# Kernel optimization log

Measured on AMD Instinct MI355X. Metric: run time of the kernel, lower is better.

## Reference

```python
import jax, jax.numpy as jnp
import numpy as np

B, T, C = 2, 2048, 2048
H, D, G = 16, 128, 4   # num_heads, head_dim, num_kv_groups
EPS = 1e-6


def setup_inputs() -> dict:
    key = jax.random.key(0)
    ks = jax.random.split(key, 6)
    x = jax.random.normal(ks[0], (B, T, C), dtype=jnp.float32)
    # causal mask: True = disallowed (strictly upper triangular)
    mask = jnp.triu(jnp.ones((T, T), dtype=bool), k=1)
    # RoPE tables, full head_dim with duplicated angle halves
    inv_freq = 1.0 / (10000.0 ** (jnp.arange(0, D, 2, dtype=jnp.float32) / D))
    angles = jnp.arange(T, dtype=jnp.float32)[:, None] * inv_freq[None, :]  # [T, D/2]
    angles = jnp.concatenate([angles, angles], axis=-1)                     # [T, D]
    cos, sin = jnp.cos(angles), jnp.sin(angles)
    std = 0.02
    W_query = jax.random.normal(ks[1], (C, H * D), dtype=jnp.float32) * std
    W_key = jax.random.normal(ks[2], (C, G * D), dtype=jnp.float32) * std
    W_value = jax.random.normal(ks[3], (C, G * D), dtype=jnp.float32) * std
    W_out = jax.random.normal(ks[4], (H * D, C), dtype=jnp.float32) * std
    q_scale = jnp.ones((D,), dtype=jnp.float32)
    k_scale = jnp.ones((D,), dtype=jnp.float32)
    return {"x": x, "mask": mask, "cos": cos, "sin": sin,
            "W_query": W_query, "W_key": W_key, "W_value": W_value,
            "W_out": W_out, "q_scale": q_scale, "k_scale": k_scale}


def _rmsnorm(x, scale):
    # qwen3-compatible: compute in fp32, rescale, cast back
    xf = x.astype(jnp.float32)
    var = jnp.mean(xf * xf, axis=-1, keepdims=True)
    return (xf * jax.lax.rsqrt(var + EPS) * scale).astype(x.dtype)


def _rope(x, cos, sin):
    d = x.shape[-1]
    x1, x2 = x[..., : d // 2], x[..., d // 2 :]
    rotated = jnp.concatenate([-x2, x1], axis=-1)
    # cos/sin: [T, D] -> broadcast over [B, H, T, D]
    return (x * cos[None, None] + rotated * sin[None, None]).astype(x.dtype)


def reference(x, mask, cos, sin, W_query, W_key, W_value, W_out, q_scale, k_scale):
    b, t, _ = x.shape
    Q = (x @ W_query).reshape(b, t, H, D).transpose(0, 2, 1, 3)  # [B,H,T,D]
    K = (x @ W_key).reshape(b, t, G, D).transpose(0, 2, 1, 3)    # [B,G,T,D]
    V = (x @ W_value).reshape(b, t, G, D).transpose(0, 2, 1, 3)
    group_size = H // G
    K = jnp.repeat(K, group_size, axis=1)  # [B,H,T,D]
    V = jnp.repeat(V, group_size, axis=1)
    Q = _rmsnorm(Q, q_scale)
    K = _rmsnorm(K, k_scale)
    Q = _rope(Q, cos, sin)
    K = _rope(K, cos, sin)
    scale = D ** (-0.5)
    attn = jnp.einsum("bhqd,bhkd->bhqk", Q, K) * scale
    attn = jnp.where(mask[None, None], -jnp.inf, attn)
    w = jax.nn.softmax(attn, axis=-1)
    out = jnp.einsum("bhqk,bhkd->bhqd", w, V)
    out = out.transpose(0, 2, 1, 3).reshape(b, t, H * D)
    return out @ W_out
```

## Files before the change

kernel.cpp:

```cpp
#include <hip/hip_runtime.h>
#include <hip/hip_bf16.h>

#define Bq 2
#define Tt 2048
#define Cc 2048
#define Hh 16
#define Dd 128
#define Gg 4

using bf16 = __hip_bfloat16;
typedef __attribute__((ext_vector_type(8))) short short8;
typedef __attribute__((ext_vector_type(4))) float f32x4;

__device__ __forceinline__ void gload_lds16(const void* g, void* l) {
    __builtin_amdgcn_global_load_lds(
        (const __attribute__((address_space(1))) unsigned int*)g,
        (__attribute__((address_space(3))) unsigned int*)l, 16, 0, 0);
}

__global__ void k_cast_bf16(const float* __restrict__ in, bf16* __restrict__ out, int n4) {
    int i = blockIdx.x * blockDim.x + threadIdx.x;
    if (i >= n4) return;
    float4 v = ((const float4*)in)[i];
    union { bf16 h[4]; uint2 u; } u;
    u.h[0] = __float2bfloat16(v.x);
    u.h[1] = __float2bfloat16(v.y);
    u.h[2] = __float2bfloat16(v.z);
    u.h[3] = __float2bfloat16(v.w);
    ((uint2*)out)[i] = u.u;
}

__global__ void k_cast_transpose(const float* __restrict__ in, bf16* __restrict__ out,
                                 int rows, int cols, int ostride) {
    __shared__ float tile[32][33];
    int c0 = blockIdx.x * 32, r0 = blockIdx.y * 32;
    int tx = threadIdx.x, ty = threadIdx.y;
    #pragma unroll
    for (int k = 0; k < 4; ++k)
        tile[ty + 8*k][tx] = in[(size_t)(r0 + ty + 8*k) * cols + c0 + tx];
    __syncthreads();
    #pragma unroll
    for (int k = 0; k < 4; ++k)
        out[(size_t)(c0 + ty + 8*k) * ostride + r0 + tx] = __float2bfloat16(tile[tx][ty + 8*k]);
}

__global__ void k_vt(const bf16* __restrict__ QKV, bf16* __restrict__ Vt) {
    __shared__ bf16 tile[64][65];
    const int d0 = blockIdx.x * 64, t0 = blockIdx.y * 64;
    const int bg = blockIdx.z;
    const int b = bg >> 2, g = bg & 3;
    const int tx = threadIdx.x, ty = threadIdx.y;
    const bf16* src = QKV + (size_t)(b * Tt) * 3072 + 2560 + g * 128;
    #pragma unroll
    for (int k = 0; k < 8; ++k)
        tile[ty + 8*k][tx] = src[(size_t)(t0 + ty + 8*k) * 3072 + d0 + tx];
    __syncthreads();
    bf16* dst = Vt + (size_t)bg * Dd * Tt;
    #pragma unroll
    for (int k = 0; k < 8; ++k)
        dst[(size_t)(d0 + ty + 8*k) * Tt + t0 + tx] = tile[tx][ty + 8*k];
}

template<int OUTF32>
__global__ __launch_bounds__(512, 2)
void k_gemm8(const bf16* __restrict__ A, const bf16* __restrict__ Bt,
             void* __restrict__ C, int M, int N, int K, int nbx) {
    __shared__ __align__(16) bf16 As[2][256 * 64];
    __shared__ __align__(16) bf16 Bs[2][256 * 64];
    const int tid = threadIdx.x;
    const int lane = tid & 63;
    const int wid = tid >> 6;
    const int wm = wid >> 2, wn = wid & 3;

    const int nb = gridDim.x;
    const int cpx = nb >> 3;
    const int id = blockIdx.x;
    const int sid = (id & 7) * cpx + (id >> 3);
    const int bx = sid % nbx, by = sid / nbx;
    const int row0 = by * 256, col0 = bx * 256;

    const int srow = tid >> 3;
    const int NT = K >> 6;

    f32x4 acc[8][4] = {};

#define STAGE_A(bufq, tt, c) {                                              \
        const int r_ = (c) * 64 + srow;                                     \
        const int ch_ = (tid & 7) ^ (r_ & 7);                               \
        gload_lds16(A + (size_t)(row0 + r_) * K + (tt) * 64 + ch_ * 8,      \
                    &As[bufq][(c) * 4096 + wid * 512]); }
#define STAGE_B(bufq, tt, c) {                                              \
        const int r_ = (c) * 64 + srow;                                     \
        const int ch_ = (tid & 7) ^ (r_ & 7);                               \
        gload_lds16(Bt + (size_t)(col0 + r_) * K + (tt) * 64 + ch_ * 8,     \
                    &Bs[bufq][(c) * 4096 + wid * 512]); }

    #pragma unroll
    for (int c = 0; c < 4; ++c) STAGE_A(0, 0, c);
    #pragma unroll
    for (int c = 0; c < 4; ++c) STAGE_B(0, 0, c);

    for (int t = 0; t < NT; ++t) {
        const int p = t & 1, q = p ^ 1;
        const bf16* a = As[p];
        const bf16* bm = Bs[p];
        const bool pf = (t + 1 < NT);

        auto rdA = [&](int i, int kk) -> short8 {
            const int ra = wm * 128 + i * 16 + (lane & 15);
            return *(const short8*)((const char*)a + ra * 128 +
                   ((kk * 64 + (lane >> 4) * 16) ^ ((ra & 7) << 4)));
        };
        auto rdB = [&](int j, int kk) -> short8 {
            const int rb = wn * 64 + j * 16 + (lane & 15);
            return *(const short8*)((const char*)bm + rb * 128 +
                   ((kk * 64 + (lane >> 4) * 16) ^ ((rb & 7) << 4)));
        };

        if (pf) { STAGE_A(q, t + 1, 0); STAGE_A(q, t + 1, 1); }
        if (pf) asm volatile("s_waitcnt vmcnt(2)" ::: "memory");
        else    asm volatile("s_waitcnt vmcnt(0)" ::: "memory");
        __builtin_amdgcn_s_barrier();
        asm volatile("" ::: "memory");

        short8 af[4][2];
        #pragma unroll
        for (int i = 0; i < 4; ++i)
            #pragma unroll
            for (int kk = 0; kk < 2; ++kk) af[i][kk] = rdA(i, kk);
        {
            short8 bf0[2][2];
            #pragma unroll
            for (int j = 0; j < 2; ++j)
                #pragma unroll
                for (int kk = 0; kk < 2; ++kk) bf0[j][kk] = rdB(j, kk);
            __builtin_amdgcn_s_setprio(1);
            #pragma unroll
            for (int i = 0; i < 4; ++i)
                #pragma unroll
                for (int j = 0; j < 2; ++j)
                    #pragma unroll
                    for (int kk = 0; kk < 2; ++kk)
                        acc[i][j] = __builtin_amdgcn_mfma_f32_16x16x32_bf16(af[i][kk], bf0[j][kk], acc[i][j], 0, 0, 0);
            __builtin_amdgcn_s_setprio(0);
        }
        asm volatile("" ::: "memory");
        __builtin_amdgcn_s_barrier();

        {
            short8 bf1[2][2];
            #pragma unroll
            for (int j = 0; j < 2; ++j)
                #pragma unroll
                for (int kk = 0; kk < 2; ++kk) bf1[j][kk] = rdB(j + 2, kk);
            if (pf) { STAGE_A(q, t + 1, 2); STAGE_A(q, t + 1, 3); }
            asm volatile("" ::: "memory");
            __builtin_amdgcn_s_barrier();
            __builtin_amdgcn_s_setprio(1);
            #pragma unroll
            for (int i = 0; i < 4; ++i)
                #pragma unroll
                for (int j = 0; j < 2; ++j)
                    #pragma unroll
                    for (int kk = 0; kk < 2; ++kk)
                        acc[i][j + 2] = __builtin_amdgcn_mfma_f32_16x16x32_bf16(af[i][kk], bf1[j][kk], acc[i][j + 2], 0, 0, 0);
            __builtin_amdgcn_s_setprio(0);
        }
        asm volatile("" ::: "memory");
        __builtin_amdgcn_s_barrier();

        short8 ag[4][2];
        #pragma unroll
        for (int i = 0; i < 4; ++i)
            #pragma unroll
            for (int kk = 0; kk < 2; ++kk) ag[i][kk] = rdA(i + 4, kk);
        {
            short8 bf0[2][2];
            #pragma unroll
            for (int j = 0; j < 2; ++j)
                #pragma unroll
                for (int kk = 0; kk < 2; ++kk) bf0[j][kk] = rdB(j, kk);
            if (pf) { STAGE_B(q, t + 1, 0); STAGE_B(q, t + 1, 1); }
            asm volatile("" ::: "memory");
            __builtin_amdgcn_s_barrier();
            __builtin_amdgcn_s_setprio(1);
            #pragma unroll
            for (int i = 0; i < 4; ++i)
                #pragma unroll
                for (int j = 0; j < 2; ++j)
                    #pragma unroll
                    for (int kk = 0; kk < 2; ++kk)
                        acc[i + 4][j] = __builtin_amdgcn_mfma_f32_16x16x32_bf16(ag[i][kk], bf0[j][kk], acc[i + 4][j], 0, 0, 0);
            __builtin_amdgcn_s_setprio(0);
        }
        asm volatile("" ::: "memory");
        __builtin_amdgcn_s_barrier();

        {
            short8 bf1[2][2];
            #pragma unroll
            for (int j = 0; j < 2; ++j)
                #pragma unroll
                for (int kk = 0; kk < 2; ++kk) bf1[j][kk] = rdB(j + 2, kk);
            if (pf) { STAGE_B(q, t + 1, 2); STAGE_B(q, t + 1, 3); }
            asm volatile("" ::: "memory");
            __builtin_amdgcn_s_barrier();
            __builtin_amdgcn_s_setprio(1);
            #pragma unroll
            for (int i = 0; i < 4; ++i)
                #pragma unroll
                for (int j = 0; j < 2; ++j)
                    #pragma unroll
                    for (int kk = 0; kk < 2; ++kk)
                        acc[i + 4][j + 2] = __builtin_amdgcn_mfma_f32_16x16x32_bf16(ag[i][kk], bf1[j][kk], acc[i + 4][j + 2], 0, 0, 0);
            __builtin_amdgcn_s_setprio(0);
        }
        asm volatile("" ::: "memory");
        __builtin_amdgcn_s_barrier();
    }
#undef STAGE_A
#undef STAGE_B

    const int crow0 = row0 + wm * 128 + (lane >> 4) * 4;
    const int ccol0 = col0 + wn * 64 + (lane & 15);
    #pragma unroll
    for (int i = 0; i < 8; ++i)
        #pragma unroll
        for (int j = 0; j < 4; ++j)
            #pragma unroll
            for (int r = 0; r < 4; ++r) {
                const size_t idx = (size_t)(crow0 + i * 16 + r) * N + ccol0 + j * 16;
                const float v = acc[i][j][r];
                if (OUTF32) ((float*)C)[idx] = v;
                else        ((bf16*)C)[idx] = __float2bfloat16(v);
            }
}

__global__ void k_qkv_post(const bf16* __restrict__ QKV,
                           const float* __restrict__ cosT, const float* __restrict__ sinT,
                           const float* __restrict__ qs, const float* __restrict__ ks,
                           bf16* __restrict__ Qr, bf16* __restrict__ Kr) {
    const int bt = blockIdx.x;
    const int b = bt >> 11;
    const int t = bt & 2047;
    const int lane = threadIdx.x & 63;
    const int wave = threadIdx.x >> 6;
    const float c1 = cosT[t * 128 + lane],      c2 = cosT[t * 128 + 64 + lane];
    const float s1 = sinT[t * 128 + lane],      s2 = sinT[t * 128 + 64 + lane];
    const float qs1 = qs[lane], qs2 = qs[lane + 64];
    const float ks1 = ks[lane], ks2 = ks[lane + 64];
    const bf16* rowb = QKV + (size_t)bt * 3072;
    for (int rr = wave; rr < 20; rr += 4) {
        const bf16* src = rowb + rr * 128;
        const float x1 = __bfloat162float(src[lane]);
        const float x2 = __bfloat162float(src[lane + 64]);
        bf16* dst;
        if (rr < 16) dst = Qr + ((size_t)(b * Hh + rr) * Tt + t) * 128;
        else         dst = Kr + ((size_t)(b * Gg + (rr - 16)) * Tt + t) * 128;
        float ssum = x1 * x1 + x2 * x2;
        #pragma unroll
        for (int o = 32; o > 0; o >>= 1) ssum += __shfl_xor(ssum, o);
        const float inv = rsqrtf(ssum * (1.0f / 128.0f) + 1e-6f);
        const float post = (rr < 16) ? 0.08838834764831845f : 1.0f;
        const float sc1 = ((rr < 16) ? qs1 : ks1) * inv;
        const float sc2 = ((rr < 16) ? qs2 : ks2) * inv;
        const float y1 = x1 * sc1;
        const float y2 = x2 * sc2;
        dst[lane]      = __float2bfloat16((y1 * c1 - y2 * s1) * post);
        dst[lane + 64] = __float2bfloat16((y2 * c2 + y1 * s2) * post);
    }
}

__global__ __launch_bounds__(256)
void k_attn(const bf16* __restrict__ Qr, const bf16* __restrict__ Kr,
            const bf16* __restrict__ Vt, bf16* __restrict__ AO) {
    __shared__ __align__(16) bf16 Ksm[2][64 * 128];
    __shared__ __align__(16) bf16 Vsm[2][128 * 64];
    __shared__ __align__(16) bf16 Psm[4][16 * 64];
    const int id = blockIdx.x;
    const int bg = id & 7;
    const int wid = id >> 3;
    const int pair = wid & 15;
    const int hg = wid >> 4;
    const int b = bg >> 2, g = bg & 3;
    const int h = g * 4 + hg;
    const int lane = threadIdx.x & 63;
    const int wave = threadIdx.x >> 6;

    const bf16* Kbase = Kr + (size_t)(b * Gg + g) * Tt * Dd;
    const bf16* Vbase = Vt + (size_t)(b * Gg + g) * Dd * Tt;

    for (int pass = 0; pass < 2; ++pass) {
        const int qt = pass ? (31 - pair) : pair;
        const bf16* Qbase = Qr + ((size_t)(b * Hh + h) * Tt + qt * 64) * Dd;

        short8 qf[4];
        #pragma unroll
        for (int kk = 0; kk < 4; ++kk)
            qf[kk] = *(const short8*)(Qbase + (size_t)(wave * 16 + (lane & 15)) * 128 + kk * 32 + (lane >> 4) * 8);

        float l_run[4] = {0.f, 0.f, 0.f, 0.f};
        f32x4 oacc[8];
        #pragma unroll
        for (int j = 0; j < 8; ++j) oacc[j] = (f32x4){0.f, 0.f, 0.f, 0.f};

        {
            #pragma unroll
            for (int j = 0; j < 4; ++j) {
                const int c = j * 4 + wave;
                const int rtk = c * 4 + (lane >> 4);
                const int chk = (lane & 15) ^ (rtk & 7);
                gload_lds16(Kbase + (size_t)rtk * 128 + chk * 8, Ksm[0] + c * 512);
                const int rtv = c * 8 + (lane >> 3);
                const int chv = (lane & 7) ^ ((lane >> 3) & 7);
                gload_lds16(Vbase + (size_t)rtv * Tt + chv * 8, Vsm[0] + c * 512);
            }
        }

        int cur = 0;
        for (int tk = 0; tk <= qt; ++tk) {
            __syncthreads();

            if (tk < qt) {
                const int k0n = (tk + 1) * 64;
                #pragma unroll
                for (int j = 0; j < 4; ++j) {
                    const int c = j * 4 + wave;
                    const int rtk = c * 4 + (lane >> 4);
                    const int chk = (lane & 15) ^ (rtk & 7);
                    gload_lds16(Kbase + (size_t)(k0n + rtk) * 128 + chk * 8, Ksm[cur ^ 1] + c * 512);
                    const int rtv = c * 8 + (lane >> 3);
                    const int chv = (lane & 7) ^ ((lane >> 3) & 7);
                    gload_lds16(Vbase + (size_t)rtv * Tt + k0n + chv * 8, Vsm[cur ^ 1] + c * 512);
                }
            }

            const bf16* Ks = Ksm[cur];
            const bf16* Vs = Vsm[cur];

            f32x4 s[4];
            #pragma unroll
            for (int nt = 0; nt < 4; ++nt) s[nt] = (f32x4){0.f, 0.f, 0.f, 0.f};
            __builtin_amdgcn_s_setprio(1);
            #pragma unroll
            for (int nt = 0; nt < 4; ++nt) {
                #pragma unroll
                for (int kk = 0; kk < 4; ++kk) {
                    const int rk = nt * 16 + (lane & 15);
                    short8 kf = *(const short8*)((const char*)Ks + rk * 256 +
                                ((kk * 64 + (lane >> 4) * 16) ^ ((rk & 7) << 4)));
                    s[nt] = __builtin_amdgcn_mfma_f32_16x16x32_bf16(qf[kk], kf, s[nt], 0, 0, 0);
                }
            }
            __builtin_amdgcn_s_setprio(0);

            if (tk == qt) {
                const int qrow = qt * 64 + wave * 16 + (lane >> 4) * 4;
                const int k0 = tk * 64;
                #pragma unroll
                for (int nt = 0; nt < 4; ++nt) {
                    const int kcol = k0 + nt * 16 + (lane & 15);
                    #pragma unroll
                    for (int r = 0; r < 4; ++r)
                        if (kcol > qrow + r) s[nt][r] = -1e30f;
                }
            }

            #pragma unroll
            for (int nt = 0; nt < 4; ++nt)
                #pragma unroll
                for (int r = 0; r < 4; ++r) {
                    const float p = __expf(s[nt][r]);
                    l_run[r] += p;
                    s[nt][r] = p;
                }

            #pragma unroll
            for (int nt = 0; nt < 4; ++nt)
                #pragma unroll
                for (int r = 0; r < 4; ++r) {
                    const int prow = (lane >> 4) * 4 + r;
                    const int pcol = nt * 16 + (lane & 15);
                    *(bf16*)((char*)Psm[wave] + ((prow * 128 + pcol * 2) ^ ((prow & 7) << 4))) =
                        __float2bfloat16(s[nt][r]);
                }
            #pragma unroll
            for (int kk = 0; kk < 2; ++kk) {
                const int pr = lane & 15;
                short8 pf = *(const short8*)((const char*)Psm[wave] + pr * 128 +
                            ((kk * 64 + (lane >> 4) * 16) ^ ((pr & 7) << 4)));
                __builtin_amdgcn_s_setprio(1);
                #pragma unroll
                for (int j = 0; j < 8; ++j) {
                    const int rb = j * 16 + (lane & 15);
                    short8 vf = *(const short8*)((const char*)Vs + rb * 128 +
                                ((kk * 64 + (lane >> 4) * 16) ^ ((rb & 7) << 4)));
                    oacc[j] = __builtin_amdgcn_mfma_f32_16x16x32_bf16(pf, vf, oacc[j], 0, 0, 0);
                }
                __builtin_amdgcn_s_setprio(0);
            }
            cur ^= 1;
        }
        __syncthreads();

        #pragma unroll
        for (int o = 1; o < 16; o <<= 1)
            #pragma unroll
            for (int r = 0; r < 4; ++r) l_run[r] += __shfl_xor(l_run[r], o);

        #pragma unroll
        for (int r = 0; r < 4; ++r) {
            const float inv = 1.0f / l_run[r];
            const int qrow = qt * 64 + wave * 16 + (lane >> 4) * 4 + r;
            bf16* dst = AO + (size_t)(b * Tt + qrow) * 2048 + h * 128 + (lane & 15);
            #pragma unroll
            for (int j = 0; j < 8; ++j)
                dst[j * 16] = __float2bfloat16(oacc[j][r] * inv);
        }
    }
}

extern "C" void kernel_launch(void* const* d_in, const int* in_sizes, int n_in,
                              void* d_out, int out_size, void* d_ws, size_t ws_size,
                              hipStream_t stream) {
    const float* x    = (const float*)d_in[0];
    const float* cosT = (const float*)d_in[2];
    const float* sinT = (const float*)d_in[3];
    const float* Wq   = (const float*)d_in[4];
    const float* Wk   = (const float*)d_in[5];
    const float* Wv   = (const float*)d_in[6];
    const float* Wo   = (const float*)d_in[7];
    const float* qs   = (const float*)d_in[8];
    const float* ks   = (const float*)d_in[9];

    char* ws = (char*)d_ws;
    bf16* xb   = (bf16*)(ws);
    bf16* Wcat = (bf16*)(ws + 16777216);
    bf16* Wot  = (bf16*)(ws + 29360128);
    bf16* QKV  = (bf16*)(ws + 37748736);
    bf16* Qr   = (bf16*)(ws + 62914560);
    bf16* Kr   = (bf16*)(ws + 79691776);
    bf16* Vtp  = (bf16*)(ws + 83886080);
    bf16* AO   = (bf16*)(ws + 88080384);

    k_cast_bf16<<<8192, 256, 0, stream>>>(x, xb, 2097152);
    dim3 tb(32, 8);
    k_cast_transpose<<<dim3(64, 64), tb, 0, stream>>>(Wq, Wcat, 2048, 2048, 2048);
    k_cast_transpose<<<dim3(16, 64), tb, 0, stream>>>(Wk, Wcat + (size_t)2048 * 2048, 2048, 512, 2048);
    k_cast_transpose<<<dim3(16, 64), tb, 0, stream>>>(Wv, Wcat + (size_t)2560 * 2048, 2048, 512, 2048);
    k_cast_transpose<<<dim3(64, 64), tb, 0, stream>>>(Wo, Wot, 2048, 2048, 2048);

    k_gemm8<0><<<192, 512, 0, stream>>>(xb, Wcat, QKV, 4096, 3072, 2048, 12);
    k_qkv_post<<<4096, 256, 0, stream>>>(QKV, cosT, sinT, qs, ks, Qr, Kr);
    k_vt<<<dim3(2, 32, 8), dim3(64, 8), 0, stream>>>(QKV, Vtp);
    k_attn<<<512, 256, 0, stream>>>(Qr, Kr, Vtp, AO);
    k_gemm8<1><<<128, 512, 0, stream>>>(AO, Wot, d_out, 4096, 2048, 2048, 8);
}
```

Before: 237.0 us.

## Narrow GEMM N-tile to raise block count and simplify the pipeline loop

The bf16 GEMM kernel is templated on the N-tile width (NJF*64 columns). The QKV projection now uses 256x192 tiles over 256 blocks instead of 256x256 over 192, and the output projection uses 256x128 over 256 blocks instead of 128. The K-loop is also restructured: the whole next tile is prefetched at the top, all B fragments are loaded once, and then four groups of A rows are processed with a barrier after each. This is meant to fill more of the CUs and cut the barrier and interleaving overhead. In exchange, each block does less MFMA work per loaded byte, and the single wait at the top of the loop overlaps global loads with compute less tightly.

```diff
diff --git a/kernel.cpp b/kernel.cpp
--- a/kernel.cpp
+++ b/kernel.cpp
@@ -61,12 +61,12 @@
         dst[(size_t)(d0 + ty + 8*k) * Tt + t0 + tx] = tile[tx][ty + 8*k];
 }
 
-template<int OUTF32>
+template<int OUTF32, int NJF>
 __global__ __launch_bounds__(512, 2)
 void k_gemm8(const bf16* __restrict__ A, const bf16* __restrict__ Bt,
              void* __restrict__ C, int M, int N, int K, int nbx) {
     __shared__ __align__(16) bf16 As[2][256 * 64];
-    __shared__ __align__(16) bf16 Bs[2][256 * 64];
+    __shared__ __align__(16) bf16 Bs[2][NJF * 64 * 64];
     const int tid = threadIdx.x;
     const int lane = tid & 63;
     const int wid = tid >> 6;
@@ -77,12 +77,12 @@
     const int id = blockIdx.x;
     const int sid = (id & 7) * cpx + (id >> 3);
     const int bx = sid % nbx, by = sid / nbx;
-    const int row0 = by * 256, col0 = bx * 256;
+    const int row0 = by * 256, col0 = bx * (NJF * 64);
 
     const int srow = tid >> 3;
     const int NT = K >> 6;
 
-    f32x4 acc[8][4] = {};
+    f32x4 acc[8][NJF] = {};
 
 #define STAGE_A(bufq, tt, c) {                                              \
         const int r_ = (c) * 64 + srow;                                     \
@@ -98,13 +98,25 @@
     #pragma unroll
     for (int c = 0; c < 4; ++c) STAGE_A(0, 0, c);
     #pragma unroll
-    for (int c = 0; c < 4; ++c) STAGE_B(0, 0, c);
+    for (int c = 0; c < NJF; ++c) STAGE_B(0, 0, c);
 
     for (int t = 0; t < NT; ++t) {
         const int p = t & 1, q = p ^ 1;
         const bf16* a = As[p];
         const bf16* bm = Bs[p];
         const bool pf = (t + 1 < NT);
+
+        if (pf) {
+            #pragma unroll
+            for (int c = 0; c < 4; ++c) STAGE_A(q, t + 1, c);
+            #pragma unroll
+            for (int c = 0; c < NJF; ++c) STAGE_B(q, t + 1, c);
+            asm volatile("s_waitcnt vmcnt(%0)" :: "i"(4 + NJF) : "memory");
+        } else {
+            asm volatile("s_waitcnt vmcnt(0)" ::: "memory");
+        }
+        __builtin_amdgcn_s_barrier();
+        asm volatile("" ::: "memory");
 
         auto rdA = [&](int i, int kk) -> short8 {
             const int ra = wm * 128 + i * 16 + (lane & 15);
@@ -112,121 +124,47 @@
                    ((kk * 64 + (lane >> 4) * 16) ^ ((ra & 7) << 4)));
         };
         auto rdB = [&](int j, int kk) -> short8 {
-            const int rb = wn * 64 + j * 16 + (lane & 15);
+            const int rb = wn * (NJF * 16) + j * 16 + (lane & 15);
             return *(const short8*)((const char*)bm + rb * 128 +
                    ((kk * 64 + (lane >> 4) * 16) ^ ((rb & 7) << 4)));
         };
 
-        if (pf) { STAGE_A(q, t + 1, 0); STAGE_A(q, t + 1, 1); }
-        if (pf) asm volatile("s_waitcnt vmcnt(2)" ::: "memory");
-        else    asm volatile("s_waitcnt vmcnt(0)" ::: "memory");
-        __builtin_amdgcn_s_barrier();
-        asm volatile("" ::: "memory");
-
-        short8 af[4][2];
-        #pragma unroll
-        for (int i = 0; i < 4; ++i)
-            #pragma unroll
-            for (int kk = 0; kk < 2; ++kk) af[i][kk] = rdA(i, kk);
-        {
-            short8 bf0[2][2];
-            #pragma unroll
-            for (int j = 0; j < 2; ++j)
-                #pragma unroll
-                for (int kk = 0; kk < 2; ++kk) bf0[j][kk] = rdB(j, kk);
+        short8 bfr[NJF][2];
+        #pragma unroll
+        for (int j = 0; j < NJF; ++j)
+            #pragma unroll
+            for (int kk = 0; kk < 2; ++kk) bfr[j][kk] = rdB(j, kk);
+
+        #pragma unroll
+        for (int g = 0; g < 4; ++g) {
+            short8 af[2][2];
+            #pragma unroll
+            for (int ii = 0; ii < 2; ++ii)
+                #pragma unroll
+                for (int kk = 0; kk < 2; ++kk) af[ii][kk] = rdA(g * 2 + ii, kk);
             __builtin_amdgcn_s_setprio(1);
             #pragma unroll
-            for (int i = 0; i < 4; ++i)
-                #pragma unroll
-                for (int j = 0; j < 2; ++j)
+            for (int ii = 0; ii < 2; ++ii)
+                #pragma unroll
+                for (int j = 0; j < NJF; ++j)
                     #pragma unroll
                     for (int kk = 0; kk < 2; ++kk)
-                        acc[i][j] = __builtin_amdgcn_mfma_f32_16x16x32_bf16(af[i][kk], bf0[j][kk], acc[i][j], 0, 0, 0);
+                        acc[g * 2 + ii][j] = __builtin_amdgcn_mfma_f32_16x16x32_bf16(
+                            af[ii][kk], bfr[j][kk], acc[g * 2 + ii][j], 0, 0, 0);
             __builtin_amdgcn_s_setprio(0);
-        }
-        asm volatile("" ::: "memory");
-        __builtin_amdgcn_s_barrier();
-
-        {
-            short8 bf1[2][2];
-            #pragma unroll
-            for (int j = 0; j < 2; ++j)
-                #pragma unroll
-                for (int kk = 0; kk < 2; ++kk) bf1[j][kk] = rdB(j + 2, kk);
-            if (pf) { STAGE_A(q, t + 1, 2); STAGE_A(q, t + 1, 3); }
             asm volatile("" ::: "memory");
             __builtin_amdgcn_s_barrier();
-            __builtin_amdgcn_s_setprio(1);
-            #pragma unroll
-            for (int i = 0; i < 4; ++i)
-                #pragma unroll
-                for (int j = 0; j < 2; ++j)
-                    #pragma unroll
-                    for (int kk = 0; kk < 2; ++kk)
-                        acc[i][j + 2] = __builtin_amdgcn_mfma_f32_16x16x32_bf16(af[i][kk], bf1[j][kk], acc[i][j + 2], 0, 0, 0);
-            __builtin_amdgcn_s_setprio(0);
-        }
-        asm volatile("" ::: "memory");
-        __builtin_amdgcn_s_barrier();
-
-        short8 ag[4][2];
-        #pragma unroll
-        for (int i = 0; i < 4; ++i)
-            #pragma unroll
-            for (int kk = 0; kk < 2; ++kk) ag[i][kk] = rdA(i + 4, kk);
-        {
-            short8 bf0[2][2];
-            #pragma unroll
-            for (int j = 0; j < 2; ++j)
-                #pragma unroll
-                for (int kk = 0; kk < 2; ++kk) bf0[j][kk] = rdB(j, kk);
-            if (pf) { STAGE_B(q, t + 1, 0); STAGE_B(q, t + 1, 1); }
-            asm volatile("" ::: "memory");
-            __builtin_amdgcn_s_barrier();
-            __builtin_amdgcn_s_setprio(1);
-            #pragma unroll
-            for (int i = 0; i < 4; ++i)
-                #pragma unroll
-                for (int j = 0; j < 2; ++j)
-                    #pragma unroll
-                    for (int kk = 0; kk < 2; ++kk)
-                        acc[i + 4][j] = __builtin_amdgcn_mfma_f32_16x16x32_bf16(ag[i][kk], bf0[j][kk], acc[i + 4][j], 0, 0, 0);
-            __builtin_amdgcn_s_setprio(0);
-        }
-        asm volatile("" ::: "memory");
-        __builtin_amdgcn_s_barrier();
-
-        {
-            short8 bf1[2][2];
-            #pragma unroll
-            for (int j = 0; j < 2; ++j)
-                #pragma unroll
-                for (int kk = 0; kk < 2; ++kk) bf1[j][kk] = rdB(j + 2, kk);
-            if (pf) { STAGE_B(q, t + 1, 2); STAGE_B(q, t + 1, 3); }
-            asm volatile("" ::: "memory");
-            __builtin_amdgcn_s_barrier();
-            __builtin_amdgcn_s_setprio(1);
-            #pragma unroll
-            for (int i = 0; i < 4; ++i)
-                #pragma unroll
-                for (int j = 0; j < 2; ++j)
-                    #pragma unroll
-                    for (int kk = 0; kk < 2; ++kk)
-                        acc[i + 4][j + 2] = __builtin_amdgcn_mfma_f32_16x16x32_bf16(ag[i][kk], bf1[j][kk], acc[i + 4][j + 2], 0, 0, 0);
-            __builtin_amdgcn_s_setprio(0);
-        }
-        asm volatile("" ::: "memory");
-        __builtin_amdgcn_s_barrier();
+        }
     }
 #undef STAGE_A
 #undef STAGE_B
 
     const int crow0 = row0 + wm * 128 + (lane >> 4) * 4;
-    const int ccol0 = col0 + wn * 64 + (lane & 15);
+    const int ccol0 = col0 + wn * (NJF * 16) + (lane & 15);
     #pragma unroll
     for (int i = 0; i < 8; ++i)
         #pragma unroll
-        for (int j = 0; j < 4; ++j)
+        for (int j = 0; j < NJF; ++j)
             #pragma unroll
             for (int r = 0; r < 4; ++r) {
                 const size_t idx = (size_t)(crow0 + i * 16 + r) * N + ccol0 + j * 16;
@@ -450,9 +388,9 @@
     k_cast_transpose<<<dim3(16, 64), tb, 0, stream>>>(Wv, Wcat + (size_t)2560 * 2048, 2048, 512, 2048);
     k_cast_transpose<<<dim3(64, 64), tb, 0, stream>>>(Wo, Wot, 2048, 2048, 2048);
 
-    k_gemm8<0><<<192, 512, 0, stream>>>(xb, Wcat, QKV, 4096, 3072, 2048, 12);
+    k_gemm8<0, 3><<<256, 512, 0, stream>>>(xb, Wcat, QKV, 4096, 3072, 2048, 16);
     k_qkv_post<<<4096, 256, 0, stream>>>(QKV, cosT, sinT, qs, ks, Qr, Kr);
     k_vt<<<dim3(2, 32, 8), dim3(64, 8), 0, stream>>>(QKV, Vtp);
     k_attn<<<512, 256, 0, stream>>>(Qr, Kr, Vtp, AO);
-    k_gemm8<1><<<128, 512, 0, stream>>>(AO, Wot, d_out, 4096, 2048, 2048, 8);
-}
+    k_gemm8<1, 2><<<256, 512, 0, stream>>>(AO, Wot, d_out, 4096, 2048, 2048, 16);
+}
```

Result: faster. 209.6 us (-11.6%).
